# Performance work log

Hardware: AMD Instinct MI355X
Metric: run time of the kernel (lower is better)

Reference implementation:

```python
import jax, jax.numpy as jnp
import numpy as np

H, D = 4, 64          # n_heads, feats_per_head (hidden_size = H*D = 256)
NEG_SLOPE = 0.2       # DGL GATv2Conv default negative_slope

N_GT, N_UBS, N_AG = 100000, 20000, 20000
E_SEEN, E_NEAR = 320000, 160000
F_GT, F_UBS, F_AG = 8, 8, 16
HID = H * D


def _linear_params(key, fan_in, fan_out):
    kw, kb = jax.random.split(key)
    s = 1.0 / np.sqrt(fan_in)
    W = jax.random.uniform(kw, (fan_in, fan_out), jnp.float32, -s, s)
    b = jax.random.uniform(kb, (fan_out,), jnp.float32, -s, s)
    return W, b


def setup_inputs() -> dict:
    key = jax.random.key(0)
    ks = jax.random.split(key, 16)
    inp = {
        'x_gt': jax.random.normal(ks[0], (N_GT, F_GT), jnp.float32),
        'x_ubs': jax.random.normal(ks[1], (N_UBS, F_UBS), jnp.float32),
        'x_agent': jax.random.normal(ks[2], (N_AG, F_AG), jnp.float32),
        'seen_src': jax.random.randint(ks[3], (E_SEEN,), 0, N_GT, jnp.int32),
        'seen_dst': jax.random.randint(ks[4], (E_SEEN,), 0, N_AG, jnp.int32),
        'near_src': jax.random.randint(ks[5], (E_NEAR,), 0, N_UBS, jnp.int32),
        'near_dst': jax.random.randint(ks[6], (E_NEAR,), 0, N_AG, jnp.int32),
    }
    # GATv2Conv 'seen': (gt -> agent)
    inp['Ws_seen'], inp['bs_seen'] = _linear_params(ks[7], F_GT, HID)
    inp['Wd_seen'], inp['bd_seen'] = _linear_params(ks[8], F_AG, HID)
    inp['attn_seen'] = jax.random.normal(ks[9], (H, D), jnp.float32) * 0.1
    inp['Wr_seen'], inp['br_seen'] = _linear_params(ks[10], F_AG, HID)
    # GATv2Conv 'near': (ubs -> agent)
    inp['Ws_near'], inp['bs_near'] = _linear_params(ks[11], F_UBS, HID)
    inp['Wd_near'], inp['bd_near'] = _linear_params(ks[12], F_AG, HID)
    inp['attn_near'] = jax.random.normal(ks[13], (H, D), jnp.float32) * 0.1
    inp['Wr_near'], inp['br_near'] = _linear_params(ks[14], F_AG, HID)
    # aggregation MLP: Linear(2*HID, HID) + ReLU
    inp['W_aggr'], inp['b_aggr'] = _linear_params(ks[15], 2 * HID, HID)
    return inp


def _gatv2(h_src, h_dst, src, dst, Ws, bs, Wd, bd, attn, Wr, br, n_dst):
    # DGL GATv2Conv, bipartite, residual=True, allow_zero_in_degree, ReLU activation
    fs = (h_src @ Ws + bs).reshape(-1, H, D)   # [Ns,H,D]
    fd = (h_dst @ Wd + bd).reshape(-1, H, D)   # [Nd,H,D]
    e = jax.nn.leaky_relu(fs[src] + fd[dst], NEG_SLOPE)     # [E,H,D]
    scores = jnp.einsum('ehd,hd->eh', e, attn)              # [E,H]
    # edge softmax over incoming edges of each dst node
    m = jax.ops.segment_max(scores, dst, num_segments=n_dst)
    m = jnp.where(jnp.isfinite(m), m, 0.0)                  # zero-in-degree guard
    ex = jnp.exp(scores - m[dst])
    denom = jax.ops.segment_sum(ex, dst, num_segments=n_dst)
    alpha = ex / denom[dst]                                 # [E,H]
    rst = jax.ops.segment_sum(alpha[:, :, None] * fs[src], dst, num_segments=n_dst)
    rst = rst + (h_dst @ Wr + br).reshape(-1, H, D)         # residual
    return jax.nn.relu(rst).reshape(n_dst, H * D)


def reference(x_gt, x_ubs, x_agent, seen_src, seen_dst, near_src, near_dst,
              Ws_seen, bs_seen, Wd_seen, bd_seen, attn_seen, Wr_seen, br_seen,
              Ws_near, bs_near, Wd_near, bd_near, attn_near, Wr_near, br_near,
              W_aggr, b_aggr):
    n_ag = x_agent.shape[0]
    x1 = _gatv2(x_gt, x_agent, seen_src, seen_dst,
                Ws_seen, bs_seen, Wd_seen, bd_seen, attn_seen, Wr_seen, br_seen, n_ag)
    x2 = _gatv2(x_ubs, x_agent, near_src, near_dst,
                Ws_near, bs_near, Wd_near, bd_near, attn_near, Wr_near, br_near, n_ag)
    x_out = jnp.concatenate((x1, x2), axis=1)               # [N_ag, 2*HID]
    return jax.nn.relu(x_out @ W_aggr + b_aggr)             # [N_ag, HID]
```

## Files before the change

kernel.cpp:

```cpp
#include <hip/hip_runtime.h>
#include <math.h>

#define NEG 0.2f
#define LDSW 520
#define CAP 96

typedef short bf16x8 __attribute__((ext_vector_type(8)));
typedef float f32x4  __attribute__((ext_vector_type(4)));
typedef float f32x2  __attribute__((ext_vector_type(2)));

static __device__ __forceinline__ f32x2 pkfma(f32x2 a, f32x2 b, f32x2 c) {
    return __builtin_elementwise_fma(a, b, c);
}
static __device__ __forceinline__ f32x2 splat2(float x) { return (f32x2){x, x}; }

static __device__ __forceinline__ unsigned short f2bf(float f) {
    unsigned int x = __float_as_uint(f);
    unsigned int r = (x + 0x7FFFu + ((x >> 16) & 1u)) >> 16;
    return (unsigned short)r;
}
static __device__ __forceinline__ float rlane(float v, int l) {
    return __int_as_float(__builtin_amdgcn_readlane(__float_as_int(v), l));
}

#define DPP_ADD(x, ctrl) \
    ((x) + __int_as_float(__builtin_amdgcn_update_dpp( \
        __float_as_int(x), __float_as_int(x), (ctrl), 0xF, 0xF, true)))
static __device__ __forceinline__ float rowsum16(float v) {
    v = DPP_ADD(v, 0xB1);
    v = DPP_ADD(v, 0x4E);
    v = DPP_ADD(v, 0x141);
    v = DPP_ADD(v, 0x140);
    return v;
}

__global__ void k_hist_scatter(
    const int* __restrict__ src_s, const int* __restrict__ dst_s, int Es,
    const int* __restrict__ src_n, const int* __restrict__ dst_n, int En,
    int* __restrict__ deg_s, int* __restrict__ deg_n,
    int* __restrict__ csr_s, int* __restrict__ csr_n,
    const float* __restrict__ W, unsigned short* __restrict__ Wt)
{
    int i = blockIdx.x * 256 + threadIdx.x;
    if (i < Es) {
        int d = dst_s[i];
        int p = atomicAdd(&deg_s[d], 1);
        if (p < CAP) csr_s[d * CAP + p] = src_s[i];
    }
    int j = i - Es;
    if (j >= 0 && j < En) {
        int d = dst_n[j];
        int p = atomicAdd(&deg_n[d], 1);
        if (p < CAP) csr_n[d * CAP + p] = src_n[j];
    }
    if (i < 512 * 256) {
        int k = i >> 8, n = i & 255;
        Wt[(size_t)n * 512 + k] = f2bf(W[i]);
    }
}

#define EDGE_BODY { \
    f32x2 x0 = splat2(rlane(r0, j * 8 + 0)); \
    f32x2 x1 = splat2(rlane(r0, j * 8 + 1)); \
    f32x2 x2 = splat2(rlane(r0, j * 8 + 2)); \
    f32x2 x3 = splat2(rlane(r0, j * 8 + 3)); \
    f32x2 x4 = splat2(rlane(r0, j * 8 + 4)); \
    f32x2 x5 = splat2(rlane(r0, j * 8 + 5)); \
    f32x2 x6 = splat2(rlane(r0, j * 8 + 6)); \
    f32x2 x7 = splat2(rlane(r0, j * 8 + 7)); \
    f32x2 fs01 = bs01, fs23 = bs23; \
    fs01 = pkfma(x0, ws01[0], fs01); fs23 = pkfma(x0, ws23[0], fs23); \
    fs01 = pkfma(x1, ws01[1], fs01); fs23 = pkfma(x1, ws23[1], fs23); \
    fs01 = pkfma(x2, ws01[2], fs01); fs23 = pkfma(x2, ws23[2], fs23); \
    fs01 = pkfma(x3, ws01[3], fs01); fs23 = pkfma(x3, ws23[3], fs23); \
    fs01 = pkfma(x4, ws01[4], fs01); fs23 = pkfma(x4, ws23[4], fs23); \
    fs01 = pkfma(x5, ws01[5], fs01); fs23 = pkfma(x5, ws23[5], fs23); \
    fs01 = pkfma(x6, ws01[6], fs01); fs23 = pkfma(x6, ws23[6], fs23); \
    fs01 = pkfma(x7, ws01[7], fs01); fs23 = pkfma(x7, ws23[7], fs23); \
    f32x2 t01 = fs01 + fd01r; \
    f32x2 t23 = fs23 + fd23r; \
    t01 = __builtin_elementwise_max(t01, NEG * t01); \
    t23 = __builtin_elementwise_max(t23, NEG * t23); \
    f32x2 scp = t01 * at01; \
    scp = pkfma(t23, at23, scp); \
    float sc = scp.x + scp.y; \
    sc = rowsum16(sc); \
    float p = __expf(sc);    \
    l += p; \
    f32x2 pp = splat2(p); \
    a01 = pkfma(pp, fs01, a01); \
    a23 = pkfma(pp, fs23, a23); }

static __device__ __forceinline__ void gat_layer4(
    const float* __restrict__ x_src, const int* __restrict__ csr,
    const float* __restrict__ Ws, const float* __restrict__ bs,
    const float* __restrict__ Wd, const float* __restrict__ bd,
    const float* __restrict__ at,
    const float* __restrict__ Wr, const float* __restrict__ br,
    float xag, int lane, int w4, int nb, int n_dst,
    const int* st, const int* dg,
    const int* i1pre, const float* x0pre,
    unsigned short* __restrict__ ldsbase)
{
    const int d0 = lane * 4;
    const int gs = lane >> 3;
    const int w8 = lane & 7;

    f32x2 fd01[4], fd23[4], fr01[4], fr23[4];
    {
        float4 bdv = *(const float4*)&bd[d0];
        float4 brv = *(const float4*)&br[d0];
#pragma unroll
        for (int j = 0; j < 4; ++j) {
            fd01[j] = (f32x2){bdv.x, bdv.y}; fd23[j] = (f32x2){bdv.z, bdv.w};
            fr01[j] = (f32x2){brv.x, brv.y}; fr23[j] = (f32x2){brv.z, brv.w};
        }
#pragma unroll
        for (int k = 0; k < 16; ++k) {
            float4 wd = *(const float4*)&Wd[k * 256 + d0];
            float4 wr = *(const float4*)&Wr[k * 256 + d0];
            f32x2 wd01 = {wd.x, wd.y}, wd23 = {wd.z, wd.w};
            f32x2 wr01 = {wr.x, wr.y}, wr23 = {wr.z, wr.w};
#pragma unroll
            for (int j = 0; j < 4; ++j) {
                f32x2 xk = splat2(rlane(xag, j * 16 + k));
                fd01[j] = pkfma(xk, wd01, fd01[j]);
                fd23[j] = pkfma(xk, wd23, fd23[j]);
                fr01[j] = pkfma(xk, wr01, fr01[j]);
                fr23[j] = pkfma(xk, wr23, fr23[j]);
            }
        }
    }

    f32x2 ws01[8], ws23[8];
#pragma unroll
    for (int k = 0; k < 8; ++k) {
        float4 w = *(const float4*)&Ws[k * 256 + d0];
        ws01[k] = (f32x2){w.x, w.y};
        ws23[k] = (f32x2){w.z, w.w};
    }
    f32x2 bs01, bs23, at01, at23;
    {
        float4 b4 = *(const float4*)&bs[d0];
        float4 a4 = *(const float4*)&at[d0];
        bs01 = (f32x2){b4.x, b4.y}; bs23 = (f32x2){b4.z, b4.w};
        at01 = (f32x2){a4.x, a4.y}; at23 = (f32x2){a4.z, a4.w};
    }

#pragma unroll
    for (int rep = 0; rep < 4; ++rep) {
        const int node = nb + rep * 4 + w4;
        if (node >= n_dst) continue;

        const int start = st[rep];
        const int deg   = dg[rep];
        const f32x2 fd01r = fd01[rep], fd23r = fd23[rep];

        float l = 0.f;
        f32x2 a01 = {0.f, 0.f}, a23 = {0.f, 0.f};

        if (deg > 0) {
            float r0 = x0pre[rep];
            int   i1 = i1pre[rep];
            const int nfull = deg >> 3, tail = deg & 7;

            for (int c = 0; c < nfull; ++c) {
                float r1 = x_src[(size_t)i1 * 8 + w8];
                int e2 = c * 8 + 16 + gs; e2 = (e2 < deg) ? e2 : deg - 1;
                int i2 = csr[start + e2];
#pragma unroll
                for (int j = 0; j < 8; ++j) EDGE_BODY
                r0 = r1; i1 = i2;
            }
            if (tail) {
#pragma unroll
                for (int j = 0; j < 8; ++j)
                    if (j < tail) EDGE_BODY
            }
        }

        float inv = (l > 0.f) ? 1.f / l : 0.f;
        ushort4 o;
        o.x = f2bf(fmaxf(fmaf(a01.x, inv, fr01[rep].x), 0.f));
        o.y = f2bf(fmaxf(fmaf(a01.y, inv, fr01[rep].y), 0.f));
        o.z = f2bf(fmaxf(fmaf(a23.x, inv, fr23[rep].x), 0.f));
        o.w = f2bf(fmaxf(fmaf(a23.y, inv, fr23[rep].y), 0.f));
        *(ushort4*)(ldsbase + (rep * 4 + w4) * LDSW) = o;
    }
}

__global__ __launch_bounds__(512) void k_gatmlp(
    const float* __restrict__ xsrc_s, const int* __restrict__ deg_s_a, const int* __restrict__ csr_s,
    const float* __restrict__ Ws_s, const float* __restrict__ bs_s,
    const float* __restrict__ Wd_s, const float* __restrict__ bd_s,
    const float* __restrict__ at_s,
    const float* __restrict__ Wr_s, const float* __restrict__ br_s,
    const float* __restrict__ xsrc_n, const int* __restrict__ deg_n_a, const int* __restrict__ csr_n,
    const float* __restrict__ Ws_n, const float* __restrict__ bs_n,
    const float* __restrict__ Wd_n, const float* __restrict__ bd_n,
    const float* __restrict__ at_n,
    const float* __restrict__ Wr_n, const float* __restrict__ br_n,
    const float* __restrict__ x_ag,
    const unsigned short* __restrict__ Wt, const float* __restrict__ bmlp,
    float* __restrict__ out, int n_dst)
{
    __shared__ unsigned short xt[16 * LDSW];

    const int t = threadIdx.x;
    const int wave = t >> 6, lane = t & 63;
    const int w4 = wave & 3;
    const bool seen = wave < 4;
    const int gs = lane >> 3, w8 = lane & 7;
    const int nb = (int)blockIdx.x * 16;

    const float* x_src = seen ? xsrc_s : xsrc_n;
    const int*   degp  = seen ? deg_s_a : deg_n_a;
    const int*   csr   = seen ? csr_s  : csr_n;
    const float* Ws    = seen ? Ws_s   : Ws_n;
    const float* bs    = seen ? bs_s   : bs_n;
    const float* Wd    = seen ? Wd_s   : Wd_n;
    const float* bd    = seen ? bd_s   : bd_n;
    const float* at    = seen ? at_s   : at_n;
    const float* Wr    = seen ? Wr_s   : Wr_n;
    const float* br    = seen ? br_s   : br_n;
    const int col = seen ? 0 : 256;

    int gnode = nb + ((lane >> 4) << 2) + w4;
    int gn = (gnode < n_dst) ? gnode : (n_dst - 1);
    float xag = x_ag[(size_t)gn * 16 + (lane & 15)];

    int st[4], dg[4];
#pragma unroll
    for (int j = 0; j < 4; ++j) {
        int nd = nb + j * 4 + w4;
        nd = (nd < n_dst) ? nd : (n_dst - 1);
        int d = degp[nd];
        dg[j] = (d < CAP) ? d : CAP;
        st[j] = nd * CAP;
    }

    int i0[4], i1[4];
#pragma unroll
    for (int j = 0; j < 4; ++j) {
        int dgj = dg[j];
        if (dgj > 0) {
            int e0 = (gs < dgj) ? gs : dgj - 1;
            int e1 = (8 + gs < dgj) ? 8 + gs : dgj - 1;
            i0[j] = csr[st[j] + e0];
            i1[j] = csr[st[j] + e1];
        } else { i0[j] = 0; i1[j] = 0; }
    }
    float x0[4];
#pragma unroll
    for (int j = 0; j < 4; ++j)
        x0[j] = x_src[(size_t)i0[j] * 8 + w8];

    gat_layer4(x_src, csr, Ws, bs, Wd, bd, at, Wr, br,
               xag, lane, w4, nb, n_dst, st, dg, i1, x0, &xt[col + lane * 4]);

    __syncthreads();

    const int m16 = lane & 15, q = lane >> 4;
    const unsigned short* w0 = Wt + (size_t)(wave * 32 + m16) * 512 + q * 8;
    const unsigned short* w1 = w0 + 16 * 512;
    const unsigned short* ap = &xt[m16 * LDSW + q * 8];

    f32x4 ac0 = {0.f, 0.f, 0.f, 0.f}, ac1 = ac0;
#pragma unroll
    for (int k0 = 0; k0 < 512; k0 += 32) {
        bf16x8 a  = *(const bf16x8*)(ap + k0);
        bf16x8 b0 = *(const bf16x8*)(w0 + k0);
        bf16x8 b1 = *(const bf16x8*)(w1 + k0);
        ac0 = __builtin_amdgcn_mfma_f32_16x16x32_bf16(a, b0, ac0, 0, 0, 0);
        ac1 = __builtin_amdgcn_mfma_f32_16x16x32_bf16(a, b1, ac1, 0, 0, 0);
    }

#define EPI(AC, J) { \
        int coln = wave * 32 + (J) * 16 + m16; \
        float bv = bmlp[coln]; \
        _Pragma("unroll") \
        for (int r = 0; r < 4; ++r) { \
            int orow = nb + q * 4 + r; \
            if (orow < n_dst) \
                out[(size_t)orow * 256 + coln] = fmaxf(AC[r] + bv, 0.f); \
        } }
    EPI(ac0, 0) EPI(ac1, 1)
#undef EPI
}

extern "C" void kernel_launch(void* const* d_in, const int* in_sizes, int n_in,
                              void* d_out, int out_size, void* d_ws, size_t ws_size,
                              hipStream_t stream) {
    const float* x_gt   = (const float*)d_in[0];
    const float* x_ubs  = (const float*)d_in[1];
    const float* x_ag   = (const float*)d_in[2];
    const int* seen_src = (const int*)d_in[3];
    const int* seen_dst = (const int*)d_in[4];
    const int* near_src = (const int*)d_in[5];
    const int* near_dst = (const int*)d_in[6];
    const float* Ws_s = (const float*)d_in[7];  const float* bs_s = (const float*)d_in[8];
    const float* Wd_s = (const float*)d_in[9];  const float* bd_s = (const float*)d_in[10];
    const float* at_s = (const float*)d_in[11];
    const float* Wr_s = (const float*)d_in[12]; const float* br_s = (const float*)d_in[13];
    const float* Ws_n = (const float*)d_in[14]; const float* bs_n = (const float*)d_in[15];
    const float* Wd_n = (const float*)d_in[16]; const float* bd_n = (const float*)d_in[17];
    const float* at_n = (const float*)d_in[18];
    const float* Wr_n = (const float*)d_in[19]; const float* br_n = (const float*)d_in[20];
    const float* W_a  = (const float*)d_in[21]; const float* b_a  = (const float*)d_in[22];

    const int n_ag = in_sizes[2] / 16;
    const int E_s  = in_sizes[3];
    const int E_n  = in_sizes[5];

    char* ws = (char*)d_ws;
    int* deg_s = (int*)ws;              ws += (size_t)n_ag * 4;
    int* deg_n = (int*)ws;              ws += (size_t)n_ag * 4;
    int* csr_s = (int*)ws;              ws += (size_t)n_ag * CAP * 4;
    int* csr_n = (int*)ws;              ws += (size_t)n_ag * CAP * 4;
    unsigned short* Wt = (unsigned short*)ws;

    hipMemsetAsync(deg_s, 0, (size_t)n_ag * 8, stream);

    int gE = (E_s + E_n + 255) / 256;
    k_hist_scatter<<<gE, 256, 0, stream>>>(
        seen_src, seen_dst, E_s, near_src, near_dst, E_n,
        deg_s, deg_n, csr_s, csr_n, W_a, Wt);

    int gN = (n_ag + 15) / 16;
    k_gatmlp<<<gN, 512, 0, stream>>>(
        x_gt,  deg_s, csr_s, Ws_s, bs_s, Wd_s, bd_s, at_s, Wr_s, br_s,
        x_ubs, deg_n, csr_n, Ws_n, bs_n, Wd_n, bd_n, at_n, Wr_n, br_n,
        x_ag, Wt, b_a, (float*)d_out, n_ag);
}
```

Baseline: 256.3 us.

## Halve fused GAT+MLP block to 8 nodes and 4 waves; coalesce weight transpose writes

The fused kernel now runs 256-thread blocks covering 8 destination nodes, with two waves per edge type, instead of 512-thread blocks covering 16. Each wave takes 4 consecutive nodes and, in the MLP stage, 64 output columns using four MFMA accumulators. The aim is more, smaller blocks for better occupancy and load balance on the irregular edge loop. The cost is that half of each 16-row MFMA tile is wasted, and every block reads the full bf16 weight matrix for half as many rows. Separately, the weight transpose now writes contiguously along k and reads the fp32 source with a stride, so the stores are coalesced.

```diff
diff --git a/kernel.cpp b/kernel.cpp
--- a/kernel.cpp
+++ b/kernel.cpp
@@ -54,8 +54,8 @@
         if (p < CAP) csr_n[d * CAP + p] = src_n[j];
     }
     if (i < 512 * 256) {
-        int k = i >> 8, n = i & 255;
-        Wt[(size_t)n * 512 + k] = f2bf(W[i]);
+        int k = i & 511, n = i >> 9;
+        Wt[(size_t)n * 512 + k] = f2bf(W[k * 256 + n]);
     }
 }
 
@@ -97,10 +97,10 @@
     const float* __restrict__ Wd, const float* __restrict__ bd,
     const float* __restrict__ at,
     const float* __restrict__ Wr, const float* __restrict__ br,
-    float xag, int lane, int w4, int nb, int n_dst,
+    float xag, int lane, int nodebase, int ldsrow, int n_dst,
     const int* st, const int* dg,
     const int* i1pre, const float* x0pre,
-    unsigned short* __restrict__ ldsbase)
+    unsigned short* __restrict__ xt, int col)
 {
     const int d0 = lane * 4;
     const int gs = lane >> 3;
@@ -149,7 +149,7 @@
 
 #pragma unroll
     for (int rep = 0; rep < 4; ++rep) {
-        const int node = nb + rep * 4 + w4;
+        const int node = nodebase + rep;
         if (node >= n_dst) continue;
 
         const int start = st[rep];
@@ -185,11 +185,11 @@
         o.y = f2bf(fmaxf(fmaf(a01.y, inv, fr01[rep].y), 0.f));
         o.z = f2bf(fmaxf(fmaf(a23.x, inv, fr23[rep].x), 0.f));
         o.w = f2bf(fmaxf(fmaf(a23.y, inv, fr23[rep].y), 0.f));
-        *(ushort4*)(ldsbase + (rep * 4 + w4) * LDSW) = o;
-    }
-}
-
-__global__ __launch_bounds__(512) void k_gatmlp(
+        *(ushort4*)(&xt[(ldsrow + rep) * LDSW + col + lane * 4]) = o;
+    }
+}
+
+__global__ __launch_bounds__(256) void k_gatmlp(
     const float* __restrict__ xsrc_s, const int* __restrict__ deg_s_a, const int* __restrict__ csr_s,
     const float* __restrict__ Ws_s, const float* __restrict__ bs_s,
     const float* __restrict__ Wd_s, const float* __restrict__ bd_s,
@@ -208,10 +208,12 @@
 
     const int t = threadIdx.x;
     const int wave = t >> 6, lane = t & 63;
-    const int w4 = wave & 3;
-    const bool seen = wave < 4;
+    const bool seen = wave < 2;
+    const int w2 = wave & 1;
     const int gs = lane >> 3, w8 = lane & 7;
-    const int nb = (int)blockIdx.x * 16;
+    const int nb = (int)blockIdx.x * 8;
+    const int nodebase = nb + w2 * 4;
+    const int ldsrow = w2 * 4;
 
     const float* x_src = seen ? xsrc_s : xsrc_n;
     const int*   degp  = seen ? deg_s_a : deg_n_a;
@@ -225,14 +227,14 @@
     const float* br    = seen ? br_s   : br_n;
     const int col = seen ? 0 : 256;
 
-    int gnode = nb + ((lane >> 4) << 2) + w4;
+    int gnode = nodebase + (lane >> 4);
     int gn = (gnode < n_dst) ? gnode : (n_dst - 1);
     float xag = x_ag[(size_t)gn * 16 + (lane & 15)];
 
     int st[4], dg[4];
 #pragma unroll
     for (int j = 0; j < 4; ++j) {
-        int nd = nb + j * 4 + w4;
+        int nd = nodebase + j;
         nd = (nd < n_dst) ? nd : (n_dst - 1);
         int d = degp[nd];
         dg[j] = (d < CAP) ? d : CAP;
@@ -256,35 +258,43 @@
         x0[j] = x_src[(size_t)i0[j] * 8 + w8];
 
     gat_layer4(x_src, csr, Ws, bs, Wd, bd, at, Wr, br,
-               xag, lane, w4, nb, n_dst, st, dg, i1, x0, &xt[col + lane * 4]);
+               xag, lane, nodebase, ldsrow, n_dst, st, dg, i1, x0, xt, col);
 
     __syncthreads();
 
     const int m16 = lane & 15, q = lane >> 4;
-    const unsigned short* w0 = Wt + (size_t)(wave * 32 + m16) * 512 + q * 8;
+    const int nbase = wave * 64;
+    const unsigned short* w0 = Wt + (size_t)(nbase + m16) * 512 + q * 8;
     const unsigned short* w1 = w0 + 16 * 512;
+    const unsigned short* w2p = w0 + 32 * 512;
+    const unsigned short* w3 = w0 + 48 * 512;
     const unsigned short* ap = &xt[m16 * LDSW + q * 8];
 
-    f32x4 ac0 = {0.f, 0.f, 0.f, 0.f}, ac1 = ac0;
+    f32x4 ac0 = {0.f, 0.f, 0.f, 0.f}, ac1 = ac0, ac2 = ac0, ac3 = ac0;
 #pragma unroll
     for (int k0 = 0; k0 < 512; k0 += 32) {
         bf16x8 a  = *(const bf16x8*)(ap + k0);
         bf16x8 b0 = *(const bf16x8*)(w0 + k0);
         bf16x8 b1 = *(const bf16x8*)(w1 + k0);
+        bf16x8 b2 = *(const bf16x8*)(w2p + k0);
+        bf16x8 b3 = *(const bf16x8*)(w3 + k0);
         ac0 = __builtin_amdgcn_mfma_f32_16x16x32_bf16(a, b0, ac0, 0, 0, 0);
         ac1 = __builtin_amdgcn_mfma_f32_16x16x32_bf16(a, b1, ac1, 0, 0, 0);
+        ac2 = __builtin_amdgcn_mfma_f32_16x16x32_bf16(a, b2, ac2, 0, 0, 0);
+        ac3 = __builtin_amdgcn_mfma_f32_16x16x32_bf16(a, b3, ac3, 0, 0, 0);
     }
 
 #define EPI(AC, J) { \
-        int coln = wave * 32 + (J) * 16 + m16; \
+        int coln = nbase + (J) * 16 + m16; \
         float bv = bmlp[coln]; \
         _Pragma("unroll") \
         for (int r = 0; r < 4; ++r) { \
-            int orow = nb + q * 4 + r; \
-            if (orow < n_dst) \
+            int lrow = q * 4 + r; \
+            int orow = nb + lrow; \
+            if (lrow < 8 && orow < n_dst) \
                 out[(size_t)orow * 256 + coln] = fmaxf(AC[r] + bv, 0.f); \
         } }
-    EPI(ac0, 0) EPI(ac1, 1)
+    EPI(ac0, 0) EPI(ac1, 1) EPI(ac2, 2) EPI(ac3, 3)
 #undef EPI
 }
 
@@ -326,8 +336,8 @@
         seen_src, seen_dst, E_s, near_src, near_dst, E_n,
         deg_s, deg_n, csr_s, csr_n, W_a, Wt);
 
-    int gN = (n_ag + 15) / 16;
-    k_gatmlp<<<gN, 512, 0, stream>>>(
+    int gN = (n_ag + 7) / 8;
+    k_gatmlp<<<gN, 256, 0, stream>>>(
         x_gt,  deg_s, csr_s, Ws_s, bs_s, Wd_s, bd_s, at_s, Wr_s, br_s,
         x_ubs, deg_n, csr_n, Ws_n, bs_n, Wd_n, bd_n, at_n, Wr_n, br_n,
         x_ag, Wt, b_a, (float*)d_out, n_ag);
```

Measured after the change: 283.0 us. 10.4% more time.
